# Optimization experiments

Hardware: AMD Instinct MI355X
Metric: run time of the kernel (lower is better)

## Reference

```python
import jax, jax.numpy as jnp
import numpy as np
from jax import lax

B, CIN, H, W = 8, 3, 256, 256
CMID = 16          # conv out channels == config.in_channels
DM = 256           # d_model
P = 2              # patch size (hardcoded in Downsample)
DI = 512           # d_inner = expand * d_model
NH, HD, NS, KC = 8, 64, 128, 4   # heads, headdim, d_state, d_conv
CONVDIM = DI + 2 * NS            # 768
PROJ = 2 * DI + 2 * NS + NH      # 1288


def _sincos2d(dim, gs):
    # 2d sin-cos positional embedding, matches get_2d_sincos_pos_embed
    def emb1d(d, pos):
        omega = 1.0 / (10000.0 ** (jnp.arange(d // 2, dtype=jnp.float32) / (d / 2.0)))
        out = pos[:, None] * omega[None, :]
        return jnp.concatenate([jnp.sin(out), jnp.cos(out)], axis=1)
    g = jnp.arange(gs, dtype=jnp.float32)
    grid = jnp.stack(jnp.meshgrid(g, g), 0).reshape(2, -1)  # [2, gs*gs]
    return jnp.concatenate([emb1d(dim // 2, grid[0]), emb1d(dim // 2, grid[1])], 1)


def _mamba2(u, in_proj_w, conv1d_w, conv1d_b, dt_bias, A_log, D, norm_w, out_proj_w):
    b, l, _ = u.shape
    zxbcdt = jnp.einsum('bld,pd->blp', u, in_proj_w)              # [b,l,1288]
    z = zxbcdt[..., :DI]
    xBC = zxbcdt[..., DI:DI + CONVDIM]
    dt = zxbcdt[..., DI + CONVDIM:]                                # [b,l,NH]
    # causal depthwise conv1d over sequence, then SiLU
    xc = lax.conv_general_dilated(xBC.transpose(0, 2, 1), conv1d_w, (1,), [(KC - 1, 0)],
                                  feature_group_count=CONVDIM,
                                  dimension_numbers=('NCH', 'OIH', 'NCH'))
    xBC = jax.nn.silu(xc + conv1d_b[None, :, None]).transpose(0, 2, 1)
    xh = xBC[..., :DI].reshape(b, l, NH, HD)                       # [b,l,h,p]
    Bm = xBC[..., DI:DI + NS]                                      # [b,l,n]
    Cm = xBC[..., DI + NS:]                                        # [b,l,n]
    dt = jax.nn.softplus(dt + dt_bias)                             # [b,l,h]
    dA = jnp.exp(dt * (-jnp.exp(A_log)))                           # [b,l,h]
    dtx = dt[..., None] * xh                                       # [b,l,h,p]

    def step(s, inp):
        dtx_t, B_t, C_t, dA_t = inp
        s = s * dA_t[..., None, None] + dtx_t[..., None] * B_t[:, None, None, :]
        return s, jnp.einsum('bhpn,bn->bhp', s, C_t)

    s0 = jnp.zeros((b, NH, HD, NS), u.dtype)
    _, ys = lax.scan(step, s0, (dtx.transpose(1, 0, 2, 3), Bm.transpose(1, 0, 2),
                                Cm.transpose(1, 0, 2), dA.transpose(1, 0, 2)))
    y = ys.transpose(1, 0, 2, 3) + D[None, None, :, None] * xh     # [b,l,h,p]
    y = y.reshape(b, l, DI) * jax.nn.silu(z)                       # gated
    y = y * lax.rsqrt(jnp.mean(y * y, -1, keepdims=True) + 1e-5) * norm_w
    return jnp.einsum('bld,od->blo', y, out_proj_w)


def setup_inputs() -> dict:
    key = jax.random.key(0)
    ks = jax.random.split(key, 12)
    r = lambda i, s, sc: jax.random.normal(ks[i], s, jnp.float32) * sc
    return {
        'x': jax.random.normal(ks[0], (B, CIN, H, W), jnp.float32),
        'conv_w': r(1, (CMID, CIN, 3, 3), 0.1), 'conv_b': jnp.zeros((CMID,), jnp.float32),
        'bn_gamma': jnp.ones((CMID,), jnp.float32), 'bn_beta': jnp.zeros((CMID,), jnp.float32),
        'patch_w': r(2, (DM, CMID, P, P), 0.1), 'patch_b': jnp.zeros((DM,), jnp.float32),
        'in_proj_w': r(3, (PROJ, DM), 0.02),
        'conv1d_w': r(4, (CONVDIM, 1, KC), 0.1), 'conv1d_b': jnp.zeros((CONVDIM,), jnp.float32),
        'dt_bias': r(5, (NH,), 0.5),
        'A_log': jax.random.uniform(ks[6], (NH,), jnp.float32),
        'D': jnp.ones((NH,), jnp.float32),
        'norm_w': jnp.ones((DI,), jnp.float32),
        'out_proj_w': r(7, (DM, DI), 0.02),
        'final_w': r(8, (P * P * CMID, DM), 0.02), 'final_b': jnp.zeros((P * P * CMID,), jnp.float32),
    }


def reference(x, conv_w, conv_b, bn_gamma, bn_beta, patch_w, patch_b, in_proj_w,
              conv1d_w, conv1d_b, dt_bias, A_log, D, norm_w, out_proj_w, final_w, final_b):
    # Conv2d k=3 s=2 p=1 -> BatchNorm2d (training-mode batch stats) -> GELU
    h = lax.conv_general_dilated(x, conv_w, (2, 2), [(1, 1), (1, 1)],
                                 dimension_numbers=('NCHW', 'OIHW', 'NCHW')) + conv_b[None, :, None, None]
    mu = jnp.mean(h, (0, 2, 3), keepdims=True)
    var = jnp.var(h, (0, 2, 3), keepdims=True)
    h = (h - mu) * lax.rsqrt(var + 1e-5) * bn_gamma[None, :, None, None] + bn_beta[None, :, None, None]
    h = jax.nn.gelu(h, approximate=False)
    # PatchEmbed: conv k=p s=p, flatten to tokens, add frozen sincos pos embed
    t = lax.conv_general_dilated(h, patch_w, (P, P), 'VALID',
                                 dimension_numbers=('NCHW', 'OIHW', 'NCHW')) + patch_b[None, :, None, None]
    b, d, gh, gw = t.shape
    tok = t.reshape(b, d, gh * gw).transpose(0, 2, 1) + _sincos2d(DM, gh)[None]
    # MambaBlock: Mamba2(x) + x  (layers=1; repo loop discards all but last layer)
    y = _mamba2(tok, in_proj_w, conv1d_w, conv1d_b, dt_bias, A_log, D, norm_w, out_proj_w) + tok
    # FinalLayer: linear only (norm_final is unused in its forward)
    o = jnp.einsum('bld,od->blo', y, final_w) + final_b
    # unpatchify
    o = o.reshape(b, gh, gw, P, P, CMID)
    o = jnp.einsum('nhwpqc->nchpwq', o).reshape(b, CMID, gh * P, gw * P)
    return o
```

## Files before the change

### kernel.cpp

```cpp
#include <hip/hip_runtime.h>
#include <math.h>

#define B_  8
#define CIN 3
#define HIN 256
#define WIN 256
#define CMID 16
#define HMID 128
#define WMID 128
#define DM 256
#define L_ 4096
#define DI 512
#define NH 8
#define HD 64
#define NS 128
#define KC 4
#define CONVDIM 768
#define PROJ 1288
#define NPADIN 1408
#define MTOK (B_*L_)
#define QCH 128
#define NCH 32

typedef unsigned short bf16;
typedef __attribute__((ext_vector_type(8))) short bf16x8;
typedef __attribute__((ext_vector_type(4))) float f32x4;

__device__ inline float bf2f(bf16 u) { return __uint_as_float(((unsigned int)u) << 16); }
__device__ inline bf16 f2bf(float f) {
  unsigned int x = __float_as_uint(f);
  return (bf16)((x + 0x7fffu + ((x >> 16) & 1u)) >> 16);
}
__device__ inline unsigned int pack2bf(float a, float b) {
  return (unsigned int)f2bf(a) | ((unsigned int)f2bf(b) << 16);
}

__global__ void k_conv1(const float* __restrict__ x, const float* __restrict__ w,
                        const float* __restrict__ bias, float* __restrict__ out) {
  int idx = blockIdx.x*256 + threadIdx.x;
  if (idx >= B_*CMID*HMID*WMID) return;
  int xo = idx & 127, yo = (idx>>7)&127, co = (idx>>14)&15, b = idx>>18;
  float acc = bias[co];
  const float* xb = x + (size_t)b*CIN*HIN*WIN;
  const float* wc = w + co*CIN*9;
  #pragma unroll
  for (int ci=0; ci<CIN; ci++)
    #pragma unroll
    for (int ky=0; ky<3; ky++) {
      int yi = 2*yo - 1 + ky;
      if (yi < 0 || yi >= HIN) continue;
      #pragma unroll
      for (int kx=0; kx<3; kx++) {
        int xi = 2*xo - 1 + kx;
        if (xi < 0 || xi >= WIN) continue;
        acc += xb[(ci*HIN + yi)*WIN + xi] * wc[(ci*3+ky)*3+kx];
      }
    }
  out[idx] = acc;
}

__global__ __launch_bounds__(256) void k_bnstatsA(const float* __restrict__ h, float2* __restrict__ part) {
  int blk = blockIdx.x;
  const float4* base = (const float4*)(h + ((size_t)(blk>>2))*16384 + (blk&3)*4096);
  int tid = threadIdx.x;
  float s=0.f, s2=0.f;
  #pragma unroll
  for (int i=0;i<4;i++){
    float4 v = base[i*256 + tid];
    s += v.x+v.y+v.z+v.w;
    s2 += v.x*v.x + v.y*v.y + v.z*v.z + v.w*v.w;
  }
  #pragma unroll
  for (int off=1; off<64; off<<=1) { s += __shfl_xor(s, off); s2 += __shfl_xor(s2, off); }
  __shared__ float sb[2][4];
  if ((tid&63)==0){ sb[0][tid>>6]=s; sb[1][tid>>6]=s2; }
  __syncthreads();
  if (tid==0) part[blk] = make_float2(sb[0][0]+sb[0][1]+sb[0][2]+sb[0][3],
                                      sb[1][0]+sb[1][1]+sb[1][2]+sb[1][3]);
}

__global__ void k_bnstatsB(const float2* __restrict__ part, float* __restrict__ stats) {
  int lane = threadIdx.x;
  int c = lane >> 2, j0 = lane & 3;
  float s=0.f, s2=0.f;
  #pragma unroll
  for (int j=j0; j<32; j+=4){
    int b = j >> 2, chunk = j & 3;
    float2 p = part[(b*16+c)*4 + chunk];
    s += p.x; s2 += p.y;
  }
  s += __shfl_xor(s,1); s2 += __shfl_xor(s2,1);
  s += __shfl_xor(s,2); s2 += __shfl_xor(s2,2);
  if (j0==0){
    const float inv = 1.f/131072.f;
    float mean = s*inv;
    float var  = s2*inv - mean*mean;
    stats[c]      = mean;
    stats[16 + c] = rsqrtf(var + 1e-5f);
  }
}

__global__ __launch_bounds__(256) void k_patch(const float* __restrict__ h, const float* __restrict__ pw,
                       const float* __restrict__ pb, const float* __restrict__ stats,
                       const float* __restrict__ gamma, const float* __restrict__ beta,
                       bf16* __restrict__ tok) {
  int grp = blockIdx.x;
  int b = grp >> 9, g8 = grp & 511;
  int g0 = g8 << 3;
  int gy = g0 >> 6, gx0 = g0 & 63;
  __shared__ float sh[8][64];
  int tid = threadIdx.x;
  {
    int tk = tid >> 5, jj = (tid & 31)*2;
    int ci = jj >> 2, p = (jj >> 1) & 1;
    const float* src = &h[((size_t)(b*CMID+ci)*HMID + 2*gy+p)*WMID + 2*(gx0+tk)];
    float2 xv = *(const float2*)src;
    float mean = stats[ci], rstd = stats[16+ci];
    float sc = rstd*gamma[ci], be = beta[ci] - mean*sc;
    float v0 = xv.x*sc + be;
    float v1 = xv.y*sc + be;
    v0 = 0.5f*v0*(1.f + erff(v0*0.70710678118654752f));
    v1 = 0.5f*v1*(1.f + erff(v1*0.70710678118654752f));
    sh[tk][jj] = v0; sh[tk][jj+1] = v1;
  }
  __syncthreads();
  int d = tid;
  float wr[64];
  #pragma unroll
  for (int i4=0;i4<16;i4++) *(float4*)&wr[i4*4] = *(const float4*)&pw[d*64 + i4*4];
  float bias = pb[d];
  int i = d & 63;
  float omega = expf(-(float)i * (9.210340371976184f/64.f));
  #pragma unroll
  for (int tk=0;tk<8;tk++){
    float acc = bias;
    #pragma unroll
    for (int j=0;j<64;j++) acc = fmaf(sh[tk][j], wr[j], acc);
    float gv = (d < 128) ? (float)(gx0+tk) : (float)gy;
    float ph = gv * omega;
    float pos = (d & 64) ? __cosf(ph) : __sinf(ph);
    tok[((size_t)((b<<12) + g0 + tk))*DM + d] = f2bf(acc + pos);
  }
}

__global__ void k_cvtw(const float* __restrict__ src, bf16* __restrict__ dst,
                       int N, int kshift, int total) {
  int idx = blockIdx.x*256 + threadIdx.x;
  if (idx >= total) return;
  int n = idx >> kshift;
  dst[idx] = (n < N) ? f2bf(src[idx]) : (bf16)0;
}

template<int EPI>
__global__ __launch_bounds__(256) void k_mgemm(
    const bf16* __restrict__ A, const bf16* __restrict__ Bw, int K,
    bf16* __restrict__ o_z, bf16* __restrict__ o_x,
    bf16* __restrict__ o_y, const bf16* __restrict__ res,
    const float* __restrict__ dt_bias, const float* __restrict__ A_log,
    float* __restrict__ dtv, float* __restrict__ dAv,
    float* __restrict__ o_f, const float* __restrict__ fbias) {
  __shared__ __align__(16) bf16 sA[2][128*32];
  __shared__ __align__(16) bf16 sB[2][128*32];
  int tid = threadIdx.x;
  int lane = tid & 63, wid = tid >> 6;
  int wr = wid >> 1, wc = wid & 1;
  int m0 = blockIdx.x*128, n0 = blockIdx.y*128;
  int nk = K >> 5;
  f32x4 acc[4][4];
  #pragma unroll
  for (int i=0;i<4;i++)
    #pragma unroll
    for (int j=0;j<4;j++)
      acc[i][j] = (f32x4){0.f,0.f,0.f,0.f};

  auto stage = [&](int buf, int ks){
    int kk = ks << 5;
    #pragma unroll
    for (int i=0;i<2;i++){
      int j = i*256 + tid;
      int row = j >> 2, cc = j & 3;
      int kg = cc ^ (row & 3);
      unsigned ldsoff = (unsigned)((i*256 + wid*64) * 16);
      __builtin_amdgcn_global_load_lds(
        (const __attribute__((address_space(1))) void*)(A + (size_t)(m0+row)*K + kk + kg*8),
        (__attribute__((address_space(3))) void*)((char*)&sA[buf][0] + ldsoff), 16, 0, 0);
      __builtin_amdgcn_global_load_lds(
        (const __attribute__((address_space(1))) void*)(Bw + (size_t)(n0+row)*K + kk + kg*8),
        (__attribute__((address_space(3))) void*)((char*)&sB[buf][0] + ldsoff), 16, 0, 0);
    }
  };

  int r = lane & 15, q = lane >> 4;
  int kgo = (q ^ (r & 3)) << 3;

  stage(0, 0);
  for (int ks=0; ks<nk; ++ks){
    int cur = ks & 1;
    __syncthreads();
    if (ks+1 < nk) stage(cur^1, ks+1);
    bf16x8 af[4], bfv[4];
    #pragma unroll
    for (int a=0;a<4;a++){
      int rown = wc*64 + a*16 + r;
      af[a] = *(const bf16x8*)&sB[cur][rown*32 + kgo];
    }
    #pragma unroll
    for (int bfr=0;bfr<4;bfr++){
      int rowm = wr*64 + bfr*16 + r;
      bfv[bfr] = *(const bf16x8*)&sA[cur][rowm*32 + kgo];
    }
    #pragma unroll
    for (int a=0;a<4;a++)
      #pragma unroll
      for (int bfr=0;bfr<4;bfr++)
        acc[a][bfr] = __builtin_amdgcn_mfma_f32_16x16x32_bf16(af[a], bfv[bfr], acc[a][bfr], 0, 0, 0);
  }

  #pragma unroll
  for (int a=0;a<4;a++){
    int n4 = n0 + wc*64 + a*16 + q*4;
    #pragma unroll
    for (int bfr=0;bfr<4;bfr++){
      int m = m0 + wr*64 + bfr*16 + r;
      f32x4 v = acc[a][bfr];
      if (EPI == 0){
        if (n4 < DI) {
          *(uint2*)(o_z + (size_t)m*DI + n4) = make_uint2(pack2bf(v[0],v[1]), pack2bf(v[2],v[3]));
        } else if (n4 < DI + CONVDIM) {
          *(uint2*)(o_x + (size_t)m*CONVDIM + (n4 - DI)) = make_uint2(pack2bf(v[0],v[1]), pack2bf(v[2],v[3]));
        } else if (n4 < PROJ) {
          #pragma unroll
          for (int rr=0;rr<4;rr++){
            int hh = n4 + rr - (DI + CONVDIM);
            float xv = v[rr] + dt_bias[hh];
            float dt = (xv > 20.f) ? xv : log1pf(expf(xv));
            dtv[(size_t)m*NH + hh] = dt;
            dAv[(size_t)m*NH + hh] = expf(-expf(A_log[hh]) * dt);
          }
        }
      } else if (EPI == 1) {
        uint2 rv = *(const uint2*)(res + (size_t)m*DM + n4);
        float r0 = bf2f((bf16)(rv.x & 0xffffu)), r1 = bf2f((bf16)(rv.x >> 16));
        float r2 = bf2f((bf16)(rv.y & 0xffffu)), r3 = bf2f((bf16)(rv.y >> 16));
        *(uint2*)(o_y + (size_t)m*DM + n4) =
            make_uint2(pack2bf(v[0]+r0, v[1]+r1), pack2bf(v[2]+r2, v[3]+r3));
      } else {
        #pragma unroll
        for (int rr=0;rr<4;rr++){
          int n = n4 + rr;
          if (n < 64) {
            float vv = v[rr] + fbias[n];
            int b = m >> 12, g = m & 4095;
            int gy = g >> 6, gx = g & 63;
            int p = n >> 5, qq = (n>>4)&1, cc2 = n & 15;
            o_f[(((size_t)(b*CMID+cc2))*HMID + 2*gy+p)*WMID + (2*gx+qq)] = vv;
          }
        }
      }
    }
  }
}

__global__ __launch_bounds__(256) void k_conv1d(const bf16* __restrict__ xpre, const float* __restrict__ cw,
                         const float* __restrict__ cb, bf16* __restrict__ xbc) {
  int idx = blockIdx.x*256 + threadIdx.x;
  int gch = idx % 96;
  int tb  = idx / 96;
  int ch0 = gch*8;
  int bl0 = tb*8;
  int l0 = bl0 & (L_-1);
  float wv[32];
  #pragma unroll
  for (int i=0;i<8;i++) *(float4*)&wv[i*4] = *(const float4*)&cw[ch0*KC + i*4];
  float bs[8];
  *(float4*)&bs[0] = *(const float4*)&cb[ch0];
  *(float4*)&bs[4] = *(const float4*)&cb[ch0+4];
  uint4 rows[11];
  #pragma unroll
  for (int j=0;j<11;j++){
    int lk = l0 - 3 + j;
    if (lk < 0) rows[j] = make_uint4(0u,0u,0u,0u);
    else rows[j] = *(const uint4*)(xpre + ((size_t)bl0 - 3 + j)*CONVDIM + ch0);
  }
  #pragma unroll
  for (int t=0;t<8;t++){
    float acc[8];
    #pragma unroll
    for (int i=0;i<8;i++) acc[i] = bs[i];
    #pragma unroll
    for (int k=0;k<KC;k++){
      uint4 u = rows[t+k];
      unsigned uu[4]={u.x,u.y,u.z,u.w};
      #pragma unroll
      for (int c2=0;c2<4;c2++){
        float lo = __uint_as_float(uu[c2]<<16);
        float hi = __uint_as_float(uu[c2]&0xffff0000u);
        acc[c2*2]   = fmaf(wv[(c2*2)*4 + k],   lo, acc[c2*2]);
        acc[c2*2+1] = fmaf(wv[(c2*2+1)*4 + k], hi, acc[c2*2+1]);
      }
    }
    unsigned ou[4];
    #pragma unroll
    for (int c2=0;c2<4;c2++){
      float v0 = acc[c2*2], v1 = acc[c2*2+1];
      v0 = v0 / (1.f + __expf(-v0));
      v1 = v1 / (1.f + __expf(-v1));
      ou[c2] = pack2bf(v0, v1);
    }
    *(uint4*)(xbc + (size_t)(bl0+t)*CONVDIM + ch0) = make_uint4(ou[0],ou[1],ou[2],ou[3]);
  }
}

__global__ __launch_bounds__(512) void k_ssd1(const bf16* __restrict__ xbc,
    const float* __restrict__ dtv, const float* __restrict__ A_log,
    bf16* __restrict__ ys, bf16* __restrict__ Sst) {
  int blk = blockIdx.x;
  int c = blk & (NCH-1), h = (blk>>5)&7, b = blk>>8;
  int tid = threadIdx.x;
  int lane = tid & 63, wid = tid >> 6;
  int r = lane & 15, q = lane >> 4;
  size_t rowbase = (size_t)b*L_ + (size_t)c*QCH;
  float eA = __expf(A_log[h]);

  __shared__ __align__(16) bf16 sB[128*128];
  __shared__ __align__(16) bf16 sC[128*128];
  __shared__ __align__(16) bf16 sDX[64*128];
  __shared__ __align__(16) bf16 sBT[128*128];
  __shared__ float sDT[128];
  __shared__ float sL[128];
  __shared__ float sWS[128];
  __shared__ float sWT[2];

  #pragma unroll
  for (int i=0;i<8;i++){
    int id = i*512 + tid;
    int row = id >> 5, cg = id & 31;
    uint4 u = *(const uint4*)(xbc + (rowbase+row)*CONVDIM + DI + cg*8);
    if (cg < 16) *(uint4*)&sB[row*128 + ((cg ^ (row&15))<<3)] = u;
    else { int cg2 = cg-16; *(uint4*)&sC[row*128 + ((cg2 ^ (row&15))<<3)] = u; }
  }
  {
    int s0 = (tid >> 3)*2;
    int p0 = (tid & 7)*8;
    const bf16* x0 = xbc + (rowbase+s0)*CONVDIM + h*HD + p0;
    uint4 u0 = *(const uint4*)x0;
    uint4 u1 = *(const uint4*)(x0 + CONVDIM);
    unsigned a0[4]={u0.x,u0.y,u0.z,u0.w}, a1[4]={u1.x,u1.y,u1.z,u1.w};
    int cb2 = s0 >> 3, se = s0 & 7;
    #pragma unroll
    for (int jp=0;jp<4;jp++){
      unsigned w0=a0[jp], w1=a1[jp];
      unsigned lo = (w0 & 0xffffu) | (w1 << 16);
      unsigned hi = (w0 >> 16) | (w1 & 0xffff0000u);
      int pA = p0 + jp*2, pB = pA+1;
      *(unsigned*)&sDX[pA*128 + ((cb2 ^ (pA&15))<<3) + se] = lo;
      *(unsigned*)&sDX[pB*128 + ((cb2 ^ (pB&15))<<3) + se] = hi;
    }
  }
  if (tid < 128) sDT[tid] = dtv[(rowbase+tid)*NH + h];
  __syncthreads();

  float inc = 0.f;
  if (tid < 128){
    inc = sDT[tid];
    #pragma unroll
    for (int off=1; off<64; off<<=1){
      float u = __shfl_up(inc, off);
      if (lane >= off) inc += u;
    }
    if (lane==63) sWT[wid] = inc;
  }
  __syncthreads();
  if (tid < 128){
    if (wid==1) inc += sWT[0];
    sL[tid] = inc;
  }

  int wr = wid >> 1, wc = wid & 1;
  f32x4 accG[2][4];
  #pragma unroll
  for (int i=0;i<2;i++)
    #pragma unroll
    for (int j=0;j<4;j++) accG[i][j] = (f32x4){0.f,0.f,0.f,0.f};
  #pragma unroll
  for (int ks=0; ks<4; ks++){
    bf16x8 af[2], bfv[4];
    #pragma unroll
    for (int mf=0;mf<2;mf++){
      int s = wr*32 + mf*16 + r;
      af[mf] = *(const bf16x8*)&sB[s*128 + (((ks*4+q) ^ (s&15))<<3)];
    }
    #pragma unroll
    for (int nf=0;nf<4;nf++){
      int t = wc*64 + nf*16 + r;
      bfv[nf] = *(const bf16x8*)&sC[t*128 + (((ks*4+q) ^ (t&15))<<3)];
    }
    #pragma unroll
    for (int mf=0;mf<2;mf++)
      #pragma unroll
      for (int nf=0;nf<4;nf++)
        accG[mf][nf] = __builtin_amdgcn_mfma_f32_16x16x32_bf16(af[mf], bfv[nf], accG[mf][nf], 0, 0, 0);
  }
  __syncthreads();

  bf16* sW = sC;
  #pragma unroll
  for (int mf=0;mf<2;mf++){
    int sb4 = wr*32 + mf*16 + q*4;
    int cb4 = sb4 >> 3, se4 = sb4 & 7;
    #pragma unroll
    for (int nf=0;nf<4;nf++){
      int t = wc*64 + nf*16 + r;
      float Lt = sL[t];
      float w[4];
      #pragma unroll
      for (int rr=0;rr<4;rr++){
        int s = sb4 + rr;
        float v = 0.f;
        if (s <= t) v = accG[mf][nf][rr] * sDT[s] * __expf(-eA*(Lt - sL[s]));
        w[rr] = v;
      }
      *(uint2*)&sW[t*128 + ((cb4 ^ (t&15))<<3) + se4] =
          make_uint2(pack2bf(w[0],w[1]), pack2bf(w[2],w[3]));
    }
  }
  if (tid < 128) sWS[tid] = sDT[tid]*__expf(-eA*(sL[127]-sL[tid]));
  __syncthreads();

  {
    int n = tid >> 2, sg = tid & 3;
    #pragma unroll
    for (int i8=0;i8<4;i8++){
      unsigned short vals[8];
      #pragma unroll
      for (int j=0;j<8;j++){
        int s = sg*32 + i8*8 + j;
        float bv = bf2f(sB[s*128 + (((n>>3) ^ (s&15))<<3) + (n&7)]);
        vals[j] = f2bf(bv * sWS[s]);
      }
      int s8 = sg*4 + i8;
      *(uint4*)&sBT[n*128 + ((s8 ^ (n&15))<<3)] = *(const uint4*)vals;
    }
  }
  __syncthreads();

  {
    int wrp = wid >> 2, wct = wid & 3;
    f32x4 acc2[2][2];
    #pragma unroll
    for (int i=0;i<2;i++){ acc2[i][0]=(f32x4){0.f,0.f,0.f,0.f}; acc2[i][1]=(f32x4){0.f,0.f,0.f,0.f}; }
    #pragma unroll
    for (int ks=0; ks<4; ks++){
      bf16x8 af[2], bfv[2];
      #pragma unroll
      for (int mf=0;mf<2;mf++){
        int p = wrp*32 + mf*16 + r;
        af[mf] = *(const bf16x8*)&sDX[p*128 + (((ks*4+q) ^ (p&15))<<3)];
      }
      #pragma unroll
      for (int nf=0;nf<2;nf++){
        int t = wct*32 + nf*16 + r;
        bfv[nf] = *(const bf16x8*)&sW[t*128 + (((ks*4+q) ^ (t&15))<<3)];
      }
      #pragma unroll
      for (int mf=0;mf<2;mf++)
        #pragma unroll
        for (int nf=0;nf<2;nf++)
          acc2[mf][nf] = __builtin_amdgcn_mfma_f32_16x16x32_bf16(af[mf], bfv[nf], acc2[mf][nf], 0, 0, 0);
    }
    #pragma unroll
    for (int mf=0;mf<2;mf++){
      int pb = wrp*32 + mf*16 + q*4;
      #pragma unroll
      for (int nf=0;nf<2;nf++){
        int t = wct*32 + nf*16 + r;
        f32x4 v = acc2[mf][nf];
        *(uint2*)(ys + (rowbase+t)*DI + h*HD + pb) =
            make_uint2(pack2bf(v[0],v[1]), pack2bf(v[2],v[3]));
      }
    }
  }

  {
    int wrn = wid >> 1, wcp = wid & 1;
    f32x4 acc3[2][2];
    #pragma unroll
    for (int i=0;i<2;i++){ acc3[i][0]=(f32x4){0.f,0.f,0.f,0.f}; acc3[i][1]=(f32x4){0.f,0.f,0.f,0.f}; }
    #pragma unroll
    for (int ks=0; ks<4; ks++){
      bf16x8 af[2], bfv[2];
      #pragma unroll
      for (int mf=0;mf<2;mf++){
        int n = wrn*32 + mf*16 + r;
        af[mf] = *(const bf16x8*)&sBT[n*128 + (((ks*4+q) ^ (n&15))<<3)];
      }
      #pragma unroll
      for (int nf=0;nf<2;nf++){
        int p = wcp*32 + nf*16 + r;
        bfv[nf] = *(const bf16x8*)&sDX[p*128 + (((ks*4+q) ^ (p&15))<<3)];
      }
      #pragma unroll
      for (int mf=0;mf<2;mf++)
        #pragma unroll
        for (int nf=0;nf<2;nf++)
          acc3[mf][nf] = __builtin_amdgcn_mfma_f32_16x16x32_bf16(af[mf], bfv[nf], acc3[mf][nf], 0, 0, 0);
    }
    size_t sb = (((size_t)(b*NH+h))*NCH + c)*8192;
    #pragma unroll
    for (int mf=0;mf<2;mf++){
      int nb = wrn*32 + mf*16 + q*4;
      #pragma unroll
      for (int nf=0;nf<2;nf++){
        int p = wcp*32 + nf*16 + r;
        f32x4 v = acc3[mf][nf];
        *(uint2*)(Sst + sb + (size_t)p*128 + nb) =
            make_uint2(pack2bf(v[0],v[1]), pack2bf(v[2],v[3]));
      }
    }
  }
}

template<int NCHT, int QCHT>
__global__ __launch_bounds__(256) void k_scan2(bf16* __restrict__ Sst, const float* __restrict__ dAv) {
  constexpr int SEG = QCHT/16;
  int blk = blockIdx.x;
  int bh = blk>>2, q = blk&3;
  int b = bh>>3, h = bh&7;
  int tid = threadIdx.x;
  __shared__ float sP[NCHT];
  {
    int c = tid / SEG, seg = tid & (SEG-1);
    float prod = 1.f;
    size_t base = ((size_t)b*L_ + c*QCHT + seg*16)*NH + h;
    #pragma unroll
    for (int k=0;k<16;k++) prod *= dAv[base + (size_t)k*NH];
    #pragma unroll
    for (int off=1; off<SEG; off<<=1) prod *= __shfl_xor(prod, off);
    if (seg==0) sP[c] = prod;
  }
  __syncthreads();
  int e0 = q*2048 + tid*8;
  float acc[8];
  #pragma unroll
  for (int j=0;j<8;j++) acc[j]=0.f;
  size_t sbase = (size_t)bh*NCHT*8192 + e0;
  for (int c=0;c<NCHT;c++){
    bf16* ptr = Sst + sbase + (size_t)c*8192;
    uint4 u = *(const uint4*)ptr;
    unsigned int uu[4] = {u.x,u.y,u.z,u.w};
    float tv[8];
    #pragma unroll
    for (int k=0;k<4;k++){
      tv[2*k]   = __uint_as_float(uu[k]<<16);
      tv[2*k+1] = __uint_as_float(uu[k]&0xffff0000u);
    }
    uint4 o;
    o.x = pack2bf(acc[0],acc[1]); o.y = pack2bf(acc[2],acc[3]);
    o.z = pack2bf(acc[4],acc[5]); o.w = pack2bf(acc[6],acc[7]);
    asm volatile("s_waitcnt vmcnt(0)" ::: "memory");
    *(uint4*)ptr = o;
    float P = sP[c];
    #pragma unroll
    for (int j=0;j<8;j++) acc[j] = tv[j] + P*acc[j];
  }
}

__global__ __launch_bounds__(256) void k_ssd3(const bf16* __restrict__ xbc,
    const float* __restrict__ dtv, const float* __restrict__ A_log,
    const bf16* __restrict__ Sst, bf16* __restrict__ ys) {
  int blk = blockIdx.x;
  int c = blk & (NCH-1), h = (blk>>5)&7, b = blk>>8;
  int tid = threadIdx.x;
  int lane = tid & 63, wid = tid >> 6;
  int r = lane & 15, q = lane >> 4;
  size_t rowbase = (size_t)b*L_ + (size_t)c*QCH;
  float eA = __expf(A_log[h]);

  __shared__ __align__(16) bf16 sC[128*128];
  __shared__ float sDT[128];
  __shared__ float sAt[128];
  __shared__ float sWT[2];

  #pragma unroll
  for (int i=0;i<8;i++){
    int id = i*256 + tid;
    int row = id >> 4, cg = id & 15;
    uint4 u = *(const uint4*)(xbc + (rowbase+row)*CONVDIM + DI + NS + cg*8);
    *(uint4*)&sC[row*128 + ((cg ^ (row&15))<<3)] = u;
  }
  if (tid < 128) sDT[tid] = dtv[(rowbase+tid)*NH + h];
  __syncthreads();
  float inc = 0.f;
  if (tid < 128){
    inc = sDT[tid];
    #pragma unroll
    for (int off=1; off<64; off<<=1){
      float u = __shfl_up(inc, off);
      if (lane >= off) inc += u;
    }
    if (lane==63) sWT[wid] = inc;
  }
  __syncthreads();
  if (tid < 128){
    if (wid==1) inc += sWT[0];
    sAt[tid] = __expf(-eA*inc);
  }
  __syncthreads();

  int wrp = wid >> 1, wct = wid & 1;
  size_t sb = (((size_t)(b*NH+h))*NCH + c)*8192;
  f32x4 accP[2][4];
  #pragma unroll
  for (int i=0;i<2;i++)
    #pragma unroll
    for (int j=0;j<4;j++) accP[i][j] = (f32x4){0.f,0.f,0.f,0.f};
  #pragma unroll
  for (int ks=0; ks<4; ks++){
    bf16x8 af[2], bfv[4];
    #pragma unroll
    for (int mf=0;mf<2;mf++){
      int p = wrp*32 + mf*16 + r;
      af[mf] = *(const bf16x8*)(Sst + sb + (size_t)p*128 + ks*32 + q*8);
    }
    #pragma unroll
    for (int nf=0;nf<4;nf++){
      int t = wct*64 + nf*16 + r;
      bfv[nf] = *(const bf16x8*)&sC[t*128 + (((ks*4+q) ^ (t&15))<<3)];
    }
    #pragma unroll
    for (int mf=0;mf<2;mf++)
      #pragma unroll
      for (int nf=0;nf<4;nf++)
        accP[mf][nf] = __builtin_amdgcn_mfma_f32_16x16x32_bf16(af[mf], bfv[nf], accP[mf][nf], 0, 0, 0);
  }
  #pragma unroll
  for (int mf=0;mf<2;mf++){
    int pb = wrp*32 + mf*16 + q*4;
    #pragma unroll
    for (int nf=0;nf<4;nf++){
      int t = wct*64 + nf*16 + r;
      float at = sAt[t];
      bf16* yp = ys + (rowbase+t)*DI + h*HD + pb;
      uint2 old = *(uint2*)yp;
      float o0 = bf2f((bf16)(old.x & 0xffffu))  + at*accP[mf][nf][0];
      float o1 = bf2f((bf16)(old.x >> 16))      + at*accP[mf][nf][1];
      float o2 = bf2f((bf16)(old.y & 0xffffu))  + at*accP[mf][nf][2];
      float o3 = bf2f((bf16)(old.y >> 16))      + at*accP[mf][nf][3];
      *(uint2*)yp = make_uint2(pack2bf(o0,o1), pack2bf(o2,o3));
    }
  }
}

__global__ __launch_bounds__(256) void k_combine(bf16* __restrict__ ys, const bf16* __restrict__ xbc,
                         const bf16* __restrict__ z, const float* __restrict__ Dp,
                         const float* __restrict__ nw) {
  int bl = blockIdx.x;
  int tid = threadIdx.x;
  bf16* yrow = ys + (size_t)bl*DI;
  const bf16* xrow = xbc + (size_t)bl*CONVDIM;
  const bf16* zrow = z + (size_t)bl*DI;
  float v[2]; float ss = 0.f;
  #pragma unroll
  for (int i=0;i<2;i++) {
    int d = tid + i*256;
    float xh = bf2f(xrow[d]);
    float y = bf2f(yrow[d]) + Dp[d>>6]*xh;
    float zv = bf2f(zrow[d]);
    y *= zv / (1.f + expf(-zv));
    v[i] = y; ss += y*y;
  }
  #pragma unroll
  for (int off=1; off<64; off<<=1) ss += __shfl_xor(ss, off);
  __shared__ float sb[4];
  if ((tid&63)==0) sb[tid>>6]=ss;
  __syncthreads();
  float total = sb[0]+sb[1]+sb[2]+sb[3];
  float scale = rsqrtf(total * (1.f/512.f) + 1e-5f);
  #pragma unroll
  for (int i=0;i<2;i++) {
    int d = tid + i*256;
    yrow[d] = f2bf(v[i]*scale*nw[d]);
  }
}

extern "C" void kernel_launch(void* const* d_in, const int* in_sizes, int n_in,
                              void* d_out, int out_size, void* d_ws, size_t ws_size,
                              hipStream_t stream) {
  const float* x         = (const float*)d_in[0];
  const float* conv_w    = (const float*)d_in[1];
  const float* conv_b    = (const float*)d_in[2];
  const float* bn_gamma  = (const float*)d_in[3];
  const float* bn_beta   = (const float*)d_in[4];
  const float* patch_w   = (const float*)d_in[5];
  const float* patch_b   = (const float*)d_in[6];
  const float* in_proj_w = (const float*)d_in[7];
  const float* conv1d_w  = (const float*)d_in[8];
  const float* conv1d_b  = (const float*)d_in[9];
  const float* dt_bias   = (const float*)d_in[10];
  const float* A_log     = (const float*)d_in[11];
  const float* Dp        = (const float*)d_in[12];
  const float* norm_w    = (const float*)d_in[13];
  const float* out_proj_w= (const float*)d_in[14];
  const float* final_w   = (const float*)d_in[15];
  const float* final_b   = (const float*)d_in[16];
  float* out = (float*)d_out;

  char* Wb = (char*)d_ws;
  float* h_buf = (float*)(Wb + 0);
  bf16*  winb  = (bf16*)(Wb + 0);
  bf16*  woutb = (bf16*)(Wb + 0);
  bf16*  wfinb = (bf16*)(Wb + 262144);
  bf16*  xpost = (bf16*)(Wb + 0);
  float2* part = (float2*)(Wb + 50331648);
  bf16*  tok   = (bf16*)(Wb + 50331648);
  bf16*  zbuf  = (bf16*)(Wb + 67108864);
  bf16*  y2b   = (bf16*)(Wb + 67108864);
  bf16*  xpre  = (bf16*)(Wb + 100663296);
  bf16*  ysb   = (bf16*)(Wb + 100663296);
  bf16*  Sst   = (bf16*)(Wb + 134217728);
  float* dtv   = (float*)(Wb + 134217728 + 33554432);
  float* dAv   = dtv + 262144;
  float* stats = dAv + 262144;
  const size_t NEED = 134217728ull + 33554432 + 2097152 + 256;
  if (ws_size < NEED) {
    hipMemsetAsync(d_out, 0, (size_t)out_size*sizeof(float), stream);
    return;
  }

  k_conv1<<<dim3((B_*CMID*HMID*WMID)/256), dim3(256), 0, stream>>>(x, conv_w, conv_b, h_buf);
  k_bnstatsA<<<dim3(512), dim3(256), 0, stream>>>(h_buf, part);
  k_bnstatsB<<<dim3(1), dim3(64), 0, stream>>>(part, stats);
  k_patch<<<dim3(MTOK/8), dim3(256), 0, stream>>>(h_buf, patch_w, patch_b, stats, bn_gamma, bn_beta, tok);
  k_cvtw<<<dim3((NPADIN*DM)/256), dim3(256), 0, stream>>>(in_proj_w, winb, PROJ, 8, NPADIN*DM);
  k_mgemm<0><<<dim3(MTOK/128, NPADIN/128), dim3(256), 0, stream>>>(tok, winb, DM,
      zbuf, xpre, nullptr, nullptr, dt_bias, A_log, dtv, dAv, nullptr, nullptr);
  k_conv1d<<<dim3((MTOK/8*96)/256), dim3(256), 0, stream>>>(xpre, conv1d_w, conv1d_b, xpost);
  k_ssd1<<<dim3(B_*NH*NCH), dim3(512), 0, stream>>>(xpost, dtv, A_log, ysb, Sst);
  k_scan2<NCH,QCH><<<dim3(B_*NH*4), dim3(256), 0, stream>>>(Sst, dAv);
  k_ssd3<<<dim3(B_*NH*NCH), dim3(256), 0, stream>>>(xpost, dtv, A_log, Sst, ysb);
  k_combine<<<dim3(MTOK), dim3(256), 0, stream>>>(ysb, xpost, zbuf, Dp, norm_w);
  k_cvtw<<<dim3((DM*DI)/256), dim3(256), 0, stream>>>(out_proj_w, woutb, DM, 9, DM*DI);
  k_cvtw<<<dim3((128*DM)/256), dim3(256), 0, stream>>>(final_w, wfinb, 64, 8, 128*DM);
  k_mgemm<1><<<dim3(MTOK/128, DM/128), dim3(256), 0, stream>>>(ysb, woutb, DI,
      nullptr, nullptr, y2b, tok, nullptr, nullptr, nullptr, nullptr, nullptr, nullptr);
  k_mgemm<2><<<dim3(MTOK/128, 1), dim3(256), 0, stream>>>(y2b, wfinb, DM,
      nullptr, nullptr, nullptr, nullptr, nullptr, nullptr, nullptr, nullptr, out, final_b);
}
```

Before: 345.1 us.

## Enlarge GEMM M-tile to 256 with 512 threads and shrink ssd1 LDS footprint

The bf16 MFMA GEMM now processes a 256-row M tile with 512 threads (8 waves), staging twice the A rows per k-step while sharing one B tile. The aim is better reuse of the B tile and fewer blocks. Separately, the ssd1 kernel packs its shared buffers into one 80KB region: the transposed weighted-B matrix is built in registers and written back over sB, and sDX is loaded later into space that aliases the float scratch arrays. This removes the separate sBT buffer so more blocks can be resident per CU, at the cost of an extra barrier and more live registers (32 shorts per thread).

```diff
diff --git a/kernel.cpp b/kernel.cpp
--- a/kernel.cpp
+++ b/kernel.cpp
@@ -152,20 +152,21 @@
 }
 
 template<int EPI>
-__global__ __launch_bounds__(256) void k_mgemm(
+__global__ __launch_bounds__(512) void k_mgemm(
     const bf16* __restrict__ A, const bf16* __restrict__ Bw, int K,
     bf16* __restrict__ o_z, bf16* __restrict__ o_x,
     bf16* __restrict__ o_y, const bf16* __restrict__ res,
     const float* __restrict__ dt_bias, const float* __restrict__ A_log,
     float* __restrict__ dtv, float* __restrict__ dAv,
     float* __restrict__ o_f, const float* __restrict__ fbias) {
-  __shared__ __align__(16) bf16 sA[2][128*32];
+  __shared__ __align__(16) bf16 sA[2][256*32];
   __shared__ __align__(16) bf16 sB[2][128*32];
   int tid = threadIdx.x;
   int lane = tid & 63, wid = tid >> 6;
   int wr = wid >> 1, wc = wid & 1;
-  int m0 = blockIdx.x*128, n0 = blockIdx.y*128;
+  int m0 = blockIdx.x*256, n0 = blockIdx.y*128;
   int nk = K >> 5;
+
   f32x4 acc[4][4];
   #pragma unroll
   for (int i=0;i<4;i++)
@@ -177,13 +178,18 @@
     int kk = ks << 5;
     #pragma unroll
     for (int i=0;i<2;i++){
-      int j = i*256 + tid;
+      int j = i*512 + tid;
       int row = j >> 2, cc = j & 3;
       int kg = cc ^ (row & 3);
-      unsigned ldsoff = (unsigned)((i*256 + wid*64) * 16);
+      unsigned ldsoff = (unsigned)((i*512 + wid*64) * 16);
       __builtin_amdgcn_global_load_lds(
         (const __attribute__((address_space(1))) void*)(A + (size_t)(m0+row)*K + kk + kg*8),
         (__attribute__((address_space(3))) void*)((char*)&sA[buf][0] + ldsoff), 16, 0, 0);
+    }
+    {
+      int row = tid >> 2, cc = tid & 3;
+      int kg = cc ^ (row & 3);
+      unsigned ldsoff = (unsigned)((wid*64) * 16);
       __builtin_amdgcn_global_load_lds(
         (const __attribute__((address_space(1))) void*)(Bw + (size_t)(n0+row)*K + kk + kg*8),
         (__attribute__((address_space(3))) void*)((char*)&sB[buf][0] + ldsoff), 16, 0, 0);
@@ -322,14 +328,14 @@
   size_t rowbase = (size_t)b*L_ + (size_t)c*QCH;
   float eA = __expf(A_log[h]);
 
-  __shared__ __align__(16) bf16 sB[128*128];
-  __shared__ __align__(16) bf16 sC[128*128];
-  __shared__ __align__(16) bf16 sDX[64*128];
-  __shared__ __align__(16) bf16 sBT[128*128];
-  __shared__ float sDT[128];
-  __shared__ float sL[128];
-  __shared__ float sWS[128];
-  __shared__ float sWT[2];
+  __shared__ __align__(16) char smem[81920];
+  bf16* sB  = (bf16*)smem;
+  bf16* sC  = (bf16*)(smem + 32768);
+  bf16* sDX = (bf16*)(smem + 65536);
+  float* fDT = (float*)(smem + 65536);
+  float* fL  = fDT + 128;
+  float* fWS = fL + 128;
+  float* fWT = fWS + 128;
 
   #pragma unroll
   for (int i=0;i<8;i++){
@@ -338,6 +344,94 @@
     uint4 u = *(const uint4*)(xbc + (rowbase+row)*CONVDIM + DI + cg*8);
     if (cg < 16) *(uint4*)&sB[row*128 + ((cg ^ (row&15))<<3)] = u;
     else { int cg2 = cg-16; *(uint4*)&sC[row*128 + ((cg2 ^ (row&15))<<3)] = u; }
+  }
+  if (tid < 128) fDT[tid] = dtv[(rowbase+tid)*NH + h];
+  __syncthreads();
+
+  float inc = 0.f;
+  if (tid < 128){
+    inc = fDT[tid];
+    #pragma unroll
+    for (int off=1; off<64; off<<=1){
+      float u = __shfl_up(inc, off);
+      if (lane >= off) inc += u;
+    }
+    if (lane==63) fWT[wid] = inc;
+  }
+  __syncthreads();
+  if (tid < 128){
+    if (wid==1) inc += fWT[0];
+    fL[tid] = inc;
+  }
+
+  int wr = wid >> 1, wc = wid & 1;
+  f32x4 accG[2][4];
+  #pragma unroll
+  for (int i=0;i<2;i++)
+    #pragma unroll
+    for (int j=0;j<4;j++) accG[i][j] = (f32x4){0.f,0.f,0.f,0.f};
+  #pragma unroll
+  for (int ks=0; ks<4; ks++){
+    bf16x8 af[2], bfv[4];
+    #pragma unroll
+    for (int mf=0;mf<2;mf++){
+      int s = wr*32 + mf*16 + r;
+      af[mf] = *(const bf16x8*)&sB[s*128 + (((ks*4+q) ^ (s&15))<<3)];
+    }
+    #pragma unroll
+    for (int nf=0;nf<4;nf++){
+      int t = wc*64 + nf*16 + r;
+      bfv[nf] = *(const bf16x8*)&sC[t*128 + (((ks*4+q) ^ (t&15))<<3)];
+    }
+    #pragma unroll
+    for (int mf=0;mf<2;mf++)
+      #pragma unroll
+      for (int nf=0;nf<4;nf++)
+        accG[mf][nf] = __builtin_amdgcn_mfma_f32_16x16x32_bf16(af[mf], bfv[nf], accG[mf][nf], 0, 0, 0);
+  }
+  __syncthreads();
+
+  bf16* sW = sC;
+  #pragma unroll
+  for (int mf=0;mf<2;mf++){
+    int sb4 = wr*32 + mf*16 + q*4;
+    int cb4 = sb4 >> 3, se4 = sb4 & 7;
+    #pragma unroll
+    for (int nf=0;nf<4;nf++){
+      int t = wc*64 + nf*16 + r;
+      float Lt = fL[t];
+      float w[4];
+      #pragma unroll
+      for (int rr=0;rr<4;rr++){
+        int s = sb4 + rr;
+        float v = 0.f;
+        if (s <= t) v = accG[mf][nf][rr] * fDT[s] * __expf(-eA*(Lt - fL[s]));
+        w[rr] = v;
+      }
+      *(uint2*)&sW[t*128 + ((cb4 ^ (t&15))<<3) + se4] =
+          make_uint2(pack2bf(w[0],w[1]), pack2bf(w[2],w[3]));
+    }
+  }
+  if (tid < 128) fWS[tid] = fDT[tid]*__expf(-eA*(fL[127]-fL[tid]));
+  __syncthreads();
+
+  int nT = tid >> 2, sg = tid & 3;
+  unsigned short vals[32];
+  #pragma unroll
+  for (int i8=0;i8<4;i8++){
+    #pragma unroll
+    for (int j=0;j<8;j++){
+      int s = sg*32 + i8*8 + j;
+      float bv = bf2f(sB[s*128 + (((nT>>3) ^ (s&15))<<3) + (nT&7)]);
+      vals[i8*8+j] = f2bf(bv * fWS[s]);
+    }
+  }
+  __syncthreads();
+
+  #pragma unroll
+  for (int i8=0;i8<4;i8++){
+    int s8 = sg*4 + i8;
+    *(uint4*)&sB[nT*128 + ((s8 ^ (nT&15))<<3)] = *(const uint4*)&vals[i8*8];
   }
   {
     int s0 = (tid >> 3)*2;
@@ -357,91 +451,6 @@
       *(unsigned*)&sDX[pB*128 + ((cb2 ^ (pB&15))<<3) + se] = hi;
     }
   }
-  if (tid < 128) sDT[tid] = dtv[(rowbase+tid)*NH + h];
-  __syncthreads();
-
-  float inc = 0.f;
-  if (tid < 128){
-    inc = sDT[tid];
-    #pragma unroll
-    for (int off=1; off<64; off<<=1){
-      float u = __shfl_up(inc, off);
-      if (lane >= off) inc += u;
-    }
-    if (lane==63) sWT[wid] = inc;
-  }
-  __syncthreads();
-  if (tid < 128){
-    if (wid==1) inc += sWT[0];
-    sL[tid] = inc;
-  }
-
-  int wr = wid >> 1, wc = wid & 1;
-  f32x4 accG[2][4];
-  #pragma unroll
-  for (int i=0;i<2;i++)
-    #pragma unroll
-    for (int j=0;j<4;j++) accG[i][j] = (f32x4){0.f,0.f,0.f,0.f};
-  #pragma unroll
-  for (int ks=0; ks<4; ks++){
-    bf16x8 af[2], bfv[4];
-    #pragma unroll
-    for (int mf=0;mf<2;mf++){
-      int s = wr*32 + mf*16 + r;
-      af[mf] = *(const bf16x8*)&sB[s*128 + (((ks*4+q) ^ (s&15))<<3)];
-    }
-    #pragma unroll
-    for (int nf=0;nf<4;nf++){
-      int t = wc*64 + nf*16 + r;
-      bfv[nf] = *(const bf16x8*)&sC[t*128 + (((ks*4+q) ^ (t&15))<<3)];
-    }
-    #pragma unroll
-    for (int mf=0;mf<2;mf++)
-      #pragma unroll
-      for (int nf=0;nf<4;nf++)
-        accG[mf][nf] = __builtin_amdgcn_mfma_f32_16x16x32_bf16(af[mf], bfv[nf], accG[mf][nf], 0, 0, 0);
-  }
-  __syncthreads();
-
-  bf16* sW = sC;
-  #pragma unroll
-  for (int mf=0;mf<2;mf++){
-    int sb4 = wr*32 + mf*16 + q*4;
-    int cb4 = sb4 >> 3, se4 = sb4 & 7;
-    #pragma unroll
-    for (int nf=0;nf<4;nf++){
-      int t = wc*64 + nf*16 + r;
-      float Lt = sL[t];
-      float w[4];
-      #pragma unroll
-      for (int rr=0;rr<4;rr++){
-        int s = sb4 + rr;
-        float v = 0.f;
-        if (s <= t) v = accG[mf][nf][rr] * sDT[s] * __expf(-eA*(Lt - sL[s]));
-        w[rr] = v;
-      }
-      *(uint2*)&sW[t*128 + ((cb4 ^ (t&15))<<3) + se4] =
-          make_uint2(pack2bf(w[0],w[1]), pack2bf(w[2],w[3]));
-    }
-  }
-  if (tid < 128) sWS[tid] = sDT[tid]*__expf(-eA*(sL[127]-sL[tid]));
-  __syncthreads();
-
-  {
-    int n = tid >> 2, sg = tid & 3;
-    #pragma unroll
-    for (int i8=0;i8<4;i8++){
-      unsigned short vals[8];
-      #pragma unroll
-      for (int j=0;j<8;j++){
-        int s = sg*32 + i8*8 + j;
-        float bv = bf2f(sB[s*128 + (((n>>3) ^ (s&15))<<3) + (n&7)]);
-        vals[j] = f2bf(bv * sWS[s]);
-      }
-      int s8 = sg*4 + i8;
-      *(uint4*)&sBT[n*128 + ((s8 ^ (n&15))<<3)] = *(const uint4*)vals;
-    }
-  }
   __syncthreads();
 
   {
@@ -480,7 +489,6 @@
       }
     }
   }
-
   {
     int wrn = wid >> 1, wcp = wid & 1;
     f32x4 acc3[2][2];
@@ -492,7 +500,7 @@
       #pragma unroll
       for (int mf=0;mf<2;mf++){
         int n = wrn*32 + mf*16 + r;
-        af[mf] = *(const bf16x8*)&sBT[n*128 + (((ks*4+q) ^ (n&15))<<3)];
+        af[mf] = *(const bf16x8*)&sB[n*128 + (((ks*4+q) ^ (n&15))<<3)];
       }
       #pragma unroll
       for (int nf=0;nf<2;nf++){
@@ -732,7 +740,7 @@
   k_bnstatsB<<<dim3(1), dim3(64), 0, stream>>>(part, stats);
   k_patch<<<dim3(MTOK/8), dim3(256), 0, stream>>>(h_buf, patch_w, patch_b, stats, bn_gamma, bn_beta, tok);
   k_cvtw<<<dim3((NPADIN*DM)/256), dim3(256), 0, stream>>>(in_proj_w, winb, PROJ, 8, NPADIN*DM);
-  k_mgemm<0><<<dim3(MTOK/128, NPADIN/128), dim3(256), 0, stream>>>(tok, winb, DM,
+  k_mgemm<0><<<dim3(MTOK/256, NPADIN/128), dim3(512), 0, stream>>>(tok, winb, DM,
       zbuf, xpre, nullptr, nullptr, dt_bias, A_log, dtv, dAv, nullptr, nullptr);
   k_conv1d<<<dim3((MTOK/8*96)/256), dim3(256), 0, stream>>>(xpre, conv1d_w, conv1d_b, xpost);
   k_ssd1<<<dim3(B_*NH*NCH), dim3(512), 0, stream>>>(xpost, dtv, A_log, ysb, Sst);
@@ -741,8 +749,8 @@
   k_combine<<<dim3(MTOK), dim3(256), 0, stream>>>(ysb, xpost, zbuf, Dp, norm_w);
   k_cvtw<<<dim3((DM*DI)/256), dim3(256), 0, stream>>>(out_proj_w, woutb, DM, 9, DM*DI);
   k_cvtw<<<dim3((128*DM)/256), dim3(256), 0, stream>>>(final_w, wfinb, 64, 8, 128*DM);
-  k_mgemm<1><<<dim3(MTOK/128, DM/128), dim3(256), 0, stream>>>(ysb, woutb, DI,
+  k_mgemm<1><<<dim3(MTOK/256, DM/128), dim3(512), 0, stream>>>(ysb, woutb, DI,
       nullptr, nullptr, y2b, tok, nullptr, nullptr, nullptr, nullptr, nullptr, nullptr);
-  k_mgemm<2><<<dim3(MTOK/128, 1), dim3(256), 0, stream>>>(y2b, wfinb, DM,
+  k_mgemm<2><<<dim3(MTOK/256, 1), dim3(512), 0, stream>>>(y2b, wfinb, DM,
       nullptr, nullptr, nullptr, nullptr, nullptr, nullptr, nullptr, nullptr, out, final_b);
 }
```

Result: faster. 326.6 us (-5.4%).
